# Optimization experiments

Measured on AMD Instinct MI355X. Metric: run time of the kernel, lower is better.

Reference implementation:

```python
import jax, jax.numpy as jnp
import numpy as np

N = 20000      # nodes
E = 80000      # edges (before self loops)
NG = 64        # graphs in batch
EMB = 780      # embedding_size (768 text + 12 time)
NEG_SLOPE = 0.2
BN_EPS = 1e-5


def setup_inputs() -> dict:
    key = jax.random.key(0)
    ks = jax.random.split(key, 20)
    def rn(k, shape, s=0.05):
        return jax.random.normal(k, shape, dtype=jnp.float32) * s
    z = lambda n: jnp.zeros((n,), dtype=jnp.float32)
    o = lambda n: jnp.ones((n,), dtype=jnp.float32)
    x = jax.random.normal(ks[0], (N, 772), dtype=jnp.float32)
    edge_index = jax.random.randint(ks[1], (2, E), 0, N)
    batch = jnp.sort(jax.random.randint(ks[2], (N,), 0, NG))
    return dict(
        x=x, edge_index=edge_index, batch=batch,
        time_W=rn(ks[3], (4, 12)), time_b=z(12),
        lin_W0=rn(ks[4], (EMB, 3 * EMB)), att_src0=rn(ks[5], (3, EMB)), att_dst0=rn(ks[6], (3, EMB)),
        bias0=z(3 * EMB), gamma0=o(3 * EMB), beta0=z(3 * EMB),
        lin_W1=rn(ks[7], (3 * EMB, 3 * EMB)), att_src1=rn(ks[8], (3, EMB)), att_dst1=rn(ks[9], (3, EMB)),
        bias1=z(3 * EMB), gamma1=o(3 * EMB), beta1=z(3 * EMB),
        lin_W2=rn(ks[10], (3 * EMB, EMB)), att_src2=rn(ks[11], (1, EMB)), att_dst2=rn(ks[12], (1, EMB)),
        bias2=z(EMB), gamma2=o(EMB), beta2=z(EMB),
        mlp_W1=rn(ks[13], (EMB, 128)), mlp_b1=z(128),
        mlp_W2=rn(ks[14], (128, 64)), mlp_b2=z(64),
    )


def _gat_layer(h, src, dst, W, a_src, a_dst, b, heads):
    # PyG GATConv (eval mode: dropout off), concat=True, self loops already in src/dst
    C = W.shape[1] // heads
    hp = (h @ W).reshape(N, heads, C)                       # [N,H,C]
    a_s = jnp.sum(hp * a_src[None], axis=-1)                # [N,H]
    a_d = jnp.sum(hp * a_dst[None], axis=-1)                # [N,H]
    e = jax.nn.leaky_relu(a_s[src] + a_d[dst], NEG_SLOPE)   # [E+N,H]
    m = jax.ops.segment_max(e, dst, num_segments=N)         # segment softmax over incoming edges
    m = jnp.where(jnp.isfinite(m), m, 0.0)
    p = jnp.exp(e - m[dst])
    denom = jax.ops.segment_sum(p, dst, num_segments=N)
    alpha = p / (denom[dst] + 1e-16)                        # [E+N,H]
    out = jax.ops.segment_sum(alpha[:, :, None] * hp[src], dst, num_segments=N)  # [N,H,C]
    return out.reshape(N, heads * C) + b


def _bn(h, gamma, beta):
    # BatchNorm in training-mode math (batch statistics, biased variance)
    mu = jnp.mean(h, axis=0)
    var = jnp.mean((h - mu) ** 2, axis=0)
    return (h - mu) * jax.lax.rsqrt(var + BN_EPS) * gamma + beta


def reference(x, edge_index, batch, time_W, time_b,
              lin_W0, att_src0, att_dst0, bias0, gamma0, beta0,
              lin_W1, att_src1, att_dst1, bias1, gamma1, beta1,
              lin_W2, att_src2, att_dst2, bias2, gamma2, beta2,
              mlp_W1, mlp_b1, mlp_W2, mlp_b2):
    te = x[:, 768:772] @ time_W + time_b
    h = jnp.concatenate([jax.lax.stop_gradient(x[:, :768]), te,
                         jax.lax.stop_gradient(x[:, 772:])], axis=-1)  # [N, 780]
    sl = jnp.arange(N)
    src = jnp.concatenate([edge_index[0], sl])   # add self loops
    dst = jnp.concatenate([edge_index[1], sl])
    layers = [
        (lin_W0, att_src0, att_dst0, bias0, gamma0, beta0, 3),
        (lin_W1, att_src1, att_dst1, bias1, gamma1, beta1, 3),
        (lin_W2, att_src2, att_dst2, bias2, gamma2, beta2, 1),
    ]
    for W, a_s, a_d, b, g, bt, heads in layers:
        h = jnp.tanh(_gat_layer(h, src, dst, W, a_s, a_d, b, heads))
        h = _bn(h, g, bt)
    cnt = jax.ops.segment_sum(jnp.ones((N,), dtype=h.dtype), batch, num_segments=NG)
    pooled = jax.ops.segment_sum(h, batch, num_segments=NG) / jnp.maximum(cnt, 1.0)[:, None]
    pooled = jax.nn.relu(pooled)
    out = jnp.tanh(pooled @ mlp_W1 + mlp_b1) @ mlp_W2 + mlp_b2
    return out  # [NG, 64]
```

## Files before the change

### kernel.cpp

```cpp
#include <hip/hip_runtime.h>
#include <math.h>

#define NN   20000
#define EE   80000
#define ELP  100000
#define NGR  64
#define EMB  780
#define W3   2340
#define EMBP 832
#define W3P  2368
#define NZ   (W3+8)

static inline int cdiv_i(long long a, long long b){ return (int)((a + b - 1) / b); }

typedef _Float16 f16;
typedef _Float16 f16x4 __attribute__((ext_vector_type(4)));
typedef _Float16 f16x8 __attribute__((ext_vector_type(8)));
typedef float    f32x4 __attribute__((ext_vector_type(4)));

__device__ __forceinline__ void async_ld16(const f16* g, f16* l){
    __builtin_amdgcn_global_load_lds(
        (const __attribute__((address_space(1))) unsigned int*)g,
        (__attribute__((address_space(3))) unsigned int*)l,
        16, 0, 0);
}

__global__ void k_zero_f32(float* p, int n){
    int i = blockIdx.x*256 + threadIdx.x; if (i < n) p[i] = 0.f;
}
__global__ void k_zero_i32(int* p, int n){
    int i = blockIdx.x*256 + threadIdx.x; if (i < n) p[i] = 0;
}

__global__ void k_transpose(const float* __restrict__ W, f16* __restrict__ Wt,
                            const float* __restrict__ sc, const float* __restrict__ sh,
                            float* __restrict__ dvec, int K, int N, int KP){
    __shared__ float T[32][33];
    __shared__ float D[8][33];
    int n0 = blockIdx.x*32, k0 = blockIdx.y*32;
    int tx = threadIdx.x, ty = threadIdx.y;
    float raw[4];
#pragma unroll
    for (int r = 0; r < 4; r++){
        int k = k0 + ty + r*8;
        float w = 0.f;
        if (k < K && n0 + tx < N) w = W[(size_t)k*N + n0 + tx];
        raw[r] = w;
        T[ty + r*8][tx] = sc ? w * ((k < K) ? sc[k] : 0.f) : w;
    }
    if (sh){
        float p = 0.f;
#pragma unroll
        for (int r = 0; r < 4; r++){
            int k = k0 + ty + r*8;
            if (k < K) p += sh[k] * raw[r];
        }
        D[ty][tx] = p;
    }
    __syncthreads();
#pragma unroll
    for (int r = 0; r < 4; r++){
        int n = n0 + ty + r*8;
        int k = k0 + tx;
        if (n < N && k < KP) Wt[(size_t)n*KP + k] = (f16)T[tx][ty + r*8];
    }
    if (sh && ty == 0 && n0 + tx < N){
        float s = 0.f;
#pragma unroll
        for (int j = 0; j < 8; j++) s += D[j][tx];
        atomicAdd(&dvec[n0 + tx], s);
    }
}

__global__ void k_wvec(const float* __restrict__ W, const float* __restrict__ asrc,
                       const float* __restrict__ adst, const float* __restrict__ sc,
                       f16* __restrict__ Wt, float* __restrict__ dvec,
                       int K, int N, int KP, int H){
    int k = blockIdx.x*4 + (threadIdx.x >> 6);
    int lane = threadIdx.x & 63;
    if (k < K){
        const float* row = W + (size_t)k*N;
        float acc[6];
#pragma unroll
        for (int i = 0; i < 6; i++) acc[i] = 0.f;
        for (int c = lane; c < EMB; c += 64){
            for (int h = 0; h < H; h++){
                float wv = row[h*EMB + c];
                acc[h]     += wv * asrc[h*EMB + c];
                acc[H + h] += wv * adst[h*EMB + c];
            }
        }
        float s = sc ? sc[k] : 1.f;
        for (int i = 0; i < 2*H; i++){
            float v = acc[i];
#pragma unroll
            for (int off = 32; off; off >>= 1) v += __shfl_xor(v, off);
            if (lane == 0) Wt[(size_t)(N + i)*KP + k] = (f16)(v * s);
        }
    }
    if (blockIdx.x == 0){
        int wv = threadIdx.x >> 6;
        for (int i = wv; i < 2*H; i += 4){
            int h = (i < H) ? i : (i - H);
            const float* att = (i < H) ? (asrc + h*EMB) : (adst + h*EMB);
            float s = 0.f;
            for (int c = lane; c < EMB; c += 64) s += dvec[h*EMB + c] * att[c];
#pragma unroll
            for (int off = 32; off; off >>= 1) s += __shfl_xor(s, off);
            if (lane == 0) dvec[N + i] = s;
        }
    }
}

__global__ void k_build_h(const float* __restrict__ x, const float* __restrict__ tW,
                          const float* __restrict__ tb, f16* __restrict__ h){
    int idx = blockIdx.x*256 + threadIdx.x;
    int total = NN*(EMBP/4);
    if (idx >= total) return;
    int n = idx / (EMBP/4);
    int c0 = (idx - n*(EMBP/4))*4;
    const float* xr = x + (size_t)n*772;
    f16x4 o;
#pragma unroll
    for (int j = 0; j < 4; j++){
        int c = c0 + j; float v;
        if (c < 768) v = xr[c];
        else if (c < EMB){
            int t = c - 768;
            v = tb[t] + xr[768]*tW[t] + xr[769]*tW[12+t] + xr[770]*tW[24+t] + xr[771]*tW[36+t];
        } else v = 0.f;
        o[j] = (f16)v;
    }
    *(f16x4*)(h + (size_t)n*EMBP + c0) = o;
}

__global__ void k_deg(const int* __restrict__ ei, int* __restrict__ deg){
    int k = blockIdx.x*256 + threadIdx.x; if (k >= ELP) return;
    int d = (k < EE) ? ei[EE + k] : (k - EE);
    atomicAdd(&deg[d], 1);
}

__global__ __launch_bounds__(1024) void k_scan(int* __restrict__ deg, int* __restrict__ rp){
    __shared__ int part[1024];
    int tid = threadIdx.x;
    int i0 = tid*20;
    int n = (i0 < NN) ? min(20, NN - i0) : 0;
    int s = 0;
    for (int k = 0; k < n; k++) s += deg[i0+k];
    part[tid] = s; __syncthreads();
    for (int off = 1; off < 1024; off <<= 1){
        int t = (tid >= off) ? part[tid-off] : 0;
        __syncthreads();
        part[tid] += t;
        __syncthreads();
    }
    int run = part[tid] - s;
    for (int k = 0; k < n; k++){
        int d = deg[i0+k];
        rp[i0+k] = run;
        deg[i0+k] = run;
        run += d;
    }
    if (tid == 1023) rp[NN] = part[1023];
}

__global__ void k_fill(const int* __restrict__ ei, int* __restrict__ cursor, int* __restrict__ csrc){
    int k = blockIdx.x*256 + threadIdx.x; if (k >= ELP) return;
    int s, d;
    if (k < EE){ s = ei[k]; d = ei[EE + k]; } else { s = k - EE; d = s; }
    int pos = atomicAdd(&cursor[d], 1);
    csrc[pos] = s;
}

__global__ void k_grp(const int* __restrict__ batch, int* __restrict__ grp){
    int g = blockIdx.x*256 + threadIdx.x; if (g > NGR) return;
    int lo = 0, hi = NN;
    while (lo < hi){ int mid = (lo+hi)>>1; if (batch[mid] < g) lo = mid+1; else hi = mid; }
    grp[g] = lo;
}

__global__ __launch_bounds__(512, 4) void k_gemmT(const f16* __restrict__ A,
                                                  const f16* __restrict__ Bt,
                                                  const float* __restrict__ dvec,
                                                  f16* __restrict__ C,
                                                  float* __restrict__ a_sd,
                                                  int M, int N, int NB, int H,
                                                  int KP, int SN, int Mtiles, int NT){
    __shared__ f16 smem[36864];
    f16* sB = smem + 12288;

    int nwg = Mtiles*NT;
    int bid = blockIdx.x;
    int q = nwg >> 3, r = nwg & 7, xcd = bid & 7, lin = bid >> 3;
    int wg = (xcd < r ? xcd*(q+1) : r*(q+1) + (xcd - r)*q) + lin;
    int mt = wg / NT, nt = wg - mt*NT;
    int m0 = mt*128, n0 = nt*256;

    int tid = threadIdx.x;
    int w = tid >> 6, lane = tid & 63;
    int lm = lane & 15, lq = lane >> 4;
    int wm = w >> 2, wn = w & 3;

    int kqs = ((lane & 3) ^ ((lane >> 3) & 3)) * 8;
    const f16* gA0 = A  + (size_t)min(m0 + w*16 + (lane >> 2), M-1)*KP + kqs;
    const f16* gB0 = Bt + (size_t)min(n0 + w*32 + (lane >> 2), NB-1)*KP + kqs;
    const f16* gB1 = Bt + (size_t)min(n0 + w*32 + 16 + (lane >> 2), NB-1)*KP + kqs;
    int sa0 = w*512;
    int sb0 = w*1024, sb1 = w*1024 + 512;

    int swz  = (lq ^ ((lm >> 1) & 3)) * 8;
    int aoff = (wm*64 + lm)*32 + swz;
    int boff = (wn*64 + lm)*32 + swz;

    f32x4 acc[4][4];
#pragma unroll
    for (int i = 0; i < 4; i++)
#pragma unroll
        for (int j = 0; j < 4; j++) acc[i][j] = (f32x4)0.f;

    int KT = KP >> 5;

    async_ld16(gA0,      &smem[sa0]);
    async_ld16(gB0,      &sB[sb0]);
    async_ld16(gB1,      &sB[sb1]);
    async_ld16(gA0 + 32, &smem[4096 + sa0]);
    async_ld16(gB0 + 32, &sB[8192 + sb0]);
    async_ld16(gB1 + 32, &sB[8192 + sb1]);
    asm volatile("s_waitcnt vmcnt(3)" ::: "memory");
    __builtin_amdgcn_s_barrier();

    int cur = 0, nx2 = 2;
    for (int t = 0; t < KT; t++){
        int ac = cur*4096, bc = cur*8192;
        f16x8 aF[4], bF[4];
#pragma unroll
        for (int i = 0; i < 4; i++) aF[i] = *(const f16x8*)&smem[ac + aoff + i*512];
#pragma unroll
        for (int i = 0; i < 4; i++) bF[i] = *(const f16x8*)&sB[bc + boff + i*512];
        bool s2 = (t+2 < KT);
        if (s2){
            int ko2 = (t+2)*32;
            int a2 = nx2*4096, b2 = nx2*8192;
            async_ld16(gA0 + ko2, &smem[a2 + sa0]);
            async_ld16(gB0 + ko2, &sB[b2 + sb0]);
            async_ld16(gB1 + ko2, &sB[b2 + sb1]);
        }
        __builtin_amdgcn_s_setprio(1);
#pragma unroll
        for (int i = 0; i < 4; i++)
#pragma unroll
            for (int j = 0; j < 4; j++)
                acc[i][j] = __builtin_amdgcn_mfma_f32_16x16x32_f16(aF[i], bF[j], acc[i][j], 0, 0, 0);
        __builtin_amdgcn_s_setprio(0);
        if (s2) asm volatile("s_waitcnt vmcnt(3)" ::: "memory");
        else    asm volatile("s_waitcnt vmcnt(0)" ::: "memory");
        __builtin_amdgcn_s_barrier();
        cur = (cur == 2) ? 0 : cur + 1;
        nx2 = (nx2 == 2) ? 0 : nx2 + 1;
    }

#pragma unroll
    for (int mi = 0; mi < 4; mi++){
#pragma unroll
        for (int ni = 0; ni < 4; ni++){
            int col = n0 + wn*64 + ni*16 + lm;
            if (col >= N && col < NB){
                int jc = col - N;
                int idx = (jc < H) ? jc : (3 + jc - H);
                float dv = dvec[col];
                int rbase = m0 + wm*64 + mi*16 + lq*4;
#pragma unroll
                for (int rr = 0; rr < 4; rr++){
                    int row = rbase + rr;
                    if (row < M) a_sd[(size_t)row*6 + idx] = acc[mi][ni][rr] + dv;
                }
            }
        }
    }

    float dv4[4];
#pragma unroll
    for (int ni = 0; ni < 4; ni++){
        int gcol = n0 + wn*64 + ni*16 + lm;
        dv4[ni] = (gcol < N) ? dvec[gcol] : 0.f;
    }
    int ncols = min(256, N - n0);
#pragma unroll
    for (int mi = 0; mi < 4; mi++){
#pragma unroll
        for (int ni = 0; ni < 4; ni++){
            int colL = wn*64 + ni*16 + lm;
#pragma unroll
            for (int rr = 0; rr < 4; rr++){
                int rowL = wm*64 + mi*16 + lq*4 + rr;
                smem[rowL*264 + colL] = (f16)(acc[mi][ni][rr] + dv4[ni]);
            }
        }
    }
    asm volatile("s_waitcnt lgkmcnt(0)" ::: "memory");
    __builtin_amdgcn_s_barrier();
#pragma unroll
    for (int it = 0; it < 8; it++){
        int ch = tid + it*512;
        int rowL = ch >> 5, cc = (ch & 31)*8;
        int grow = m0 + rowL;
        if (grow < M && cc < ncols){
            if (cc + 8 <= ncols){
                f16x8 v = *(f16x8*)&smem[rowL*264 + cc];
                *(f16x8*)(C + (size_t)grow*SN + n0 + cc) = v;
            } else {
                for (int jj = cc; jj < ncols; jj++)
                    C[(size_t)grow*SN + n0 + jj] = smem[rowL*264 + jj];
            }
        }
    }
}

template<int H>
__global__ __launch_bounds__(256) void k_alpha(const int* __restrict__ rp, const int* __restrict__ csrc,
                                               const float* __restrict__ a_sd, float* __restrict__ alpha){
    int n = blockIdx.x*4 + (threadIdx.x >> 6);
    if (n >= NN) return;
    int lane = threadIdx.x & 63;
    int beg = rp[n], deg = rp[n+1] - beg;

    float adv[H];
#pragma unroll
    for (int h = 0; h < H; h++) adv[h] = a_sd[(size_t)n*6 + 3 + h];

    bool act0 = lane < deg;
    int sl0 = 0; float t0[H];
    if (act0){
        sl0 = csrc[beg + lane];
#pragma unroll
        for (int h = 0; h < H; h++){
            float t = a_sd[(size_t)sl0*6 + h] + adv[h];
            t0[h] = t > 0.f ? t : 0.2f*t;
        }
    } else {
#pragma unroll
        for (int h = 0; h < H; h++) t0[h] = -1e30f;
    }

    float mx[H];
#pragma unroll
    for (int h = 0; h < H; h++) mx[h] = t0[h];
    for (int base = 64; base < deg; base += 64){
        int e = base + lane;
        if (e < deg){
            int s = csrc[beg + e];
#pragma unroll
            for (int h = 0; h < H; h++){
                float t = a_sd[(size_t)s*6 + h] + adv[h];
                t = t > 0.f ? t : 0.2f*t;
                mx[h] = fmaxf(mx[h], t);
            }
        }
    }
#pragma unroll
    for (int off = 32; off; off >>= 1)
#pragma unroll
        for (int h = 0; h < H; h++) mx[h] = fmaxf(mx[h], __shfl_xor(mx[h], off));

    float dn[H];
#pragma unroll
    for (int h = 0; h < H; h++) dn[h] = act0 ? expf(t0[h] - mx[h]) : 0.f;
    for (int base = 64; base < deg; base += 64){
        int e = base + lane;
        if (e < deg){
            int s = csrc[beg + e];
#pragma unroll
            for (int h = 0; h < H; h++){
                float t = a_sd[(size_t)s*6 + h] + adv[h];
                t = t > 0.f ? t : 0.2f*t;
                dn[h] += expf(t - mx[h]);
            }
        }
    }
#pragma unroll
    for (int off = 32; off; off >>= 1)
#pragma unroll
        for (int h = 0; h < H; h++) dn[h] += __shfl_xor(dn[h], off);
    float inv[H];
#pragma unroll
    for (int h = 0; h < H; h++) inv[h] = 1.f / (dn[h] + 1e-16f);

    if (act0){
        if (H == 3){
            float4 o;
            o.x = expf(t0[0]-mx[0])*inv[0];
            o.y = expf(t0[1]-mx[1])*inv[1];
            o.z = expf(t0[2]-mx[2])*inv[2];
            o.w = 0.f;
            *(float4*)(alpha + (size_t)(beg+lane)*4) = o;
        } else {
            alpha[beg+lane] = expf(t0[0]-mx[0])*inv[0];
        }
    }
    for (int base = 64; base < deg; base += 64){
        int e = base + lane;
        if (e < deg){
            int s = csrc[beg + e];
            float av[H];
#pragma unroll
            for (int h = 0; h < H; h++){
                float t = a_sd[(size_t)s*6 + h] + adv[h];
                t = t > 0.f ? t : 0.2f*t;
                av[h] = expf(t - mx[h]) * inv[h];
            }
            if (H == 3){
                float4 o; o.x = av[0]; o.y = av[1]; o.z = av[2]; o.w = 0.f;
                *(float4*)(alpha + (size_t)(beg+e)*4) = o;
            } else {
                alpha[beg+e] = av[0];
            }
        }
    }
}

template<int H>
__global__ __launch_bounds__(256) void k_gather(const f16* __restrict__ hp, const int* __restrict__ rp,
                                                const int* __restrict__ csrc, const float* __restrict__ alpha,
                                                const float* __restrict__ bias, f16* __restrict__ y,
                                                int SP, int W){
    int w = threadIdx.x >> 6, lane = threadIdx.x & 63;
    int n = blockIdx.x*4 + w;
    if (n >= NN) return;
    int c = blockIdx.y*512 + lane*8;
    bool cok = c < SP;
    int beg = rp[n], deg = rp[n+1] - beg;

    int hl = 0, hh = 0, nsp = 8;
    if (H == 3){
        hl = min(c/EMB, 2); hh = min((c+7)/EMB, 2);
        nsp = (hh > hl) ? (EMB*(hl+1) - c) : 8;
    }
    float acc[8];
#pragma unroll
    for (int j = 0; j < 8; j++) acc[j] = 0.f;

    for (int base = 0; base < deg; base += 64){
        int cnt = min(64, deg - base);
        int e0 = base + lane;
        int sl = 0; float a0v = 0.f, a1v = 0.f, a2v = 0.f;
        if (e0 < deg){
            sl = csrc[beg + e0];
            if (H == 3){
                float4 al4 = *(const float4*)(alpha + (size_t)(beg+e0)*4);
                a0v = al4.x; a1v = al4.y; a2v = al4.z;
            } else {
                a0v = alpha[beg + e0];
            }
        }
#pragma unroll 4
        for (int e = 0; e < cnt; e++){
            int s = __shfl(sl, e);
            float b0 = __shfl(a0v, e);
            float b1 = (H==3) ? __shfl(a1v, e) : b0;
            float b2 = (H==3) ? __shfl(a2v, e) : b0;
            if (cok){
                f16x8 v = *(const f16x8*)(hp + (size_t)s*SP + c);
                float lo = (H==3) ? ((hl==0)?b0:((hl==1)?b1:b2)) : b0;
                float hi = (H==3) ? ((hh==0)?b0:((hh==1)?b1:b2)) : b0;
#pragma unroll
                for (int j = 0; j < 8; j++)
                    acc[j] += ((j < nsp) ? lo : hi) * (float)v[j];
            }
        }
    }

    if (cok){
        f16x8 o;
#pragma unroll
        for (int j = 0; j < 8; j++){
            float vv = (c + j < W) ? tanhf(acc[j] + bias[c+j]) : 0.f;
            o[j] = (f16)vv;
        }
        *(f16x8*)(y + (size_t)n*SP + c) = o;
    }
}

__global__ void k_bnstat(const f16* __restrict__ y, float* __restrict__ ps,
                         float* __restrict__ pq, int W, int SP){
    int c0 = (blockIdx.x*256 + threadIdx.x)*4;
    if (c0 >= W) return;
    int slice = blockIdx.y;
    int r0 = (int)(((long long)NN*slice)/128);
    int r1 = (int)(((long long)NN*(slice+1))/128);
    float s[4] = {0,0,0,0}, q[4] = {0,0,0,0};
    for (int r = r0; r < r1; r++){
        f16x4 u = *(const f16x4*)(y + (size_t)r*SP + c0);
#pragma unroll
        for (int j = 0; j < 4; j++){ float v = (float)u[j]; s[j] += v; q[j] += v*v; }
    }
#pragma unroll
    for (int j = 0; j < 4; j++){
        ps[(size_t)slice*W3 + c0+j] = s[j];
        pq[(size_t)slice*W3 + c0+j] = q[j];
    }
}

__global__ void k_bnfin(const float* __restrict__ ps, const float* __restrict__ pq,
                        const float* __restrict__ gamma, const float* __restrict__ beta,
                        float* __restrict__ sc, float* __restrict__ sh,
                        float* __restrict__ dvec, int W, int zn){
    int c = blockIdx.x*256 + threadIdx.x;
    if (c < W){
        float m = 0.f, q = 0.f;
        for (int s = 0; s < 128; s++){ m += ps[(size_t)s*W3 + c]; q += pq[(size_t)s*W3 + c]; }
        m *= (1.f/NN);
        float v = q * (1.f/NN) - m*m;
        float is = 1.f / sqrtf(v + 1e-5f);
        float g = gamma[c];
        sc[c] = is * g;
        sh[c] = beta[c] - m * is * g;
    }
    if (c < zn) dvec[c] = 0.f;
}

__global__ void k_pool(const f16* __restrict__ h, const int* __restrict__ grp,
                       float* __restrict__ pooled){
    int g = blockIdx.x;
    int c = threadIdx.x*4;
    if (c >= EMB) return;
    int r0 = grp[g], r1 = grp[g+1];
    float s0=0.f, s1=0.f, s2=0.f, s3=0.f;
    for (int r = r0; r < r1; r++){
        f16x4 u = *(const f16x4*)(h + (size_t)r*EMBP + c);
        s0 += (float)u[0]; s1 += (float)u[1]; s2 += (float)u[2]; s3 += (float)u[3];
    }
    pooled[g*EMB + c] = s0; pooled[g*EMB + c+1] = s1;
    pooled[g*EMB + c+2] = s2; pooled[g*EMB + c+3] = s3;
}

__global__ __launch_bounds__(256) void k_mlp(const float* __restrict__ pooled, const int* __restrict__ grp,
                                             const float* __restrict__ sc, const float* __restrict__ sh,
                                             const float* __restrict__ W1, const float* __restrict__ b1,
                                             const float* __restrict__ W2, const float* __restrict__ b2,
                                             float* __restrict__ out){
    __shared__ float p[EMB];
    __shared__ float hid[128];
    int g = blockIdx.x, tid = threadIdx.x;
    int cnt = grp[g+1] - grp[g];
    float ic = 1.f / fmaxf((float)cnt, 1.f);
    for (int c = tid; c < EMB; c += 256){
        float v = pooled[g*EMB + c] * ic * sc[c] + sh[c];
        p[c] = v > 0.f ? v : 0.f;
    }
    __syncthreads();
    if (tid < 128){
        float s = b1[tid];
        for (int k = 0; k < EMB; k++) s += p[k] * W1[k*128 + tid];
        hid[tid] = tanhf(s);
    }
    __syncthreads();
    if (tid < 64){
        float s = b2[tid];
        for (int k = 0; k < 128; k++) s += hid[k] * W2[k*64 + tid];
        out[g*64 + tid] = s;
    }
}

extern "C" void kernel_launch(void* const* d_in, const int* in_sizes, int n_in,
                              void* d_out, int out_size, void* d_ws, size_t ws_size,
                              hipStream_t stream) {
    (void)in_sizes; (void)n_in; (void)out_size;
    const float* x    = (const float*)d_in[0];
    const int*   ei   = (const int*)  d_in[1];
    const int*   batch= (const int*)  d_in[2];
    const float* tW   = (const float*)d_in[3];
    const float* tb   = (const float*)d_in[4];
    const float* W0   = (const float*)d_in[5];
    const float* as0  = (const float*)d_in[6];
    const float* ad0  = (const float*)d_in[7];
    const float* b0   = (const float*)d_in[8];
    const float* g0   = (const float*)d_in[9];
    const float* be0  = (const float*)d_in[10];
    const float* W1   = (const float*)d_in[11];
    const float* as1  = (const float*)d_in[12];
    const float* ad1  = (const float*)d_in[13];
    const float* b1   = (const float*)d_in[14];
    const float* g1   = (const float*)d_in[15];
    const float* be1  = (const float*)d_in[16];
    const float* W2   = (const float*)d_in[17];
    const float* as2  = (const float*)d_in[18];
    const float* ad2  = (const float*)d_in[19];
    const float* b2   = (const float*)d_in[20];
    const float* g2   = (const float*)d_in[21];
    const float* be2  = (const float*)d_in[22];
    const float* mW1  = (const float*)d_in[23];
    const float* mb1  = (const float*)d_in[24];
    const float* mW2  = (const float*)d_in[25];
    const float* mb2  = (const float*)d_in[26];
    float* outp = (float*)d_out;

    size_t off = 0;
    auto carve = [&](size_t bytes) -> void* {
        void* p = (char*)d_ws + off;
        off = (off + bytes + 255) & ~(size_t)255;
        return p;
    };
    f16* big1 = (f16*)carve((size_t)NN*W3P*2);
    f16* big2 = (f16*)carve((size_t)NN*W3P*2);
    f16* Wt   = (f16*)carve((size_t)NZ*W3P*2);
    float* a_sd  = (float*)carve((size_t)NN*6*4);
    float* psum  = (float*)carve((size_t)128*W3*4);
    float* psq   = (float*)carve((size_t)128*W3*4);
    float* sc    = (float*)carve((size_t)W3*4);
    float* sh    = (float*)carve((size_t)W3*4);
    float* dvec  = (float*)carve((size_t)NZ*4);
    float* alphab= (float*)carve((size_t)ELP*4*4);
    float* pooled= (float*)carve((size_t)NGR*EMB*4);
    int*   grp   = (int*)carve((size_t)(NGR+1)*4);
    int*   deg   = (int*)carve((size_t)NN*4);
    int*   rp    = (int*)carve((size_t)(NN+1)*4);
    int*   csrc  = (int*)carve((size_t)ELP*4);

    if (ws_size < off) return;

    k_zero_i32<<<cdiv_i(NN,256),256,0,stream>>>(deg, NN);
    k_deg<<<cdiv_i(ELP,256),256,0,stream>>>(ei, deg);
    k_scan<<<1,1024,0,stream>>>(deg, rp);
    k_fill<<<cdiv_i(ELP,256),256,0,stream>>>(ei, deg, csrc);
    k_grp<<<1,256,0,stream>>>(batch, grp);

    k_build_h<<<cdiv_i((long long)NN*(EMBP/4),256),256,0,stream>>>(x, tW, tb, big1);
    k_zero_f32<<<cdiv_i(NZ,256),256,0,stream>>>(dvec, NZ);

    struct Layer { const float* W; const float* as; const float* ad; const float* b;
                   const float* g; const float* be; int H; int K; int KP; };
    Layer layers[3] = {
        {W0, as0, ad0, b0, g0, be0, 3, EMB, EMBP},
        {W1, as1, ad1, b1, g1, be1, 3, W3,  W3P },
        {W2, as2, ad2, b2, g2, be2, 1, W3,  W3P },
    };

    for (int L = 0; L < 3; L++){
        Layer& ly = layers[L];
        int Wout  = ly.H * EMB;
        int NB    = Wout + 2*ly.H;
        int SPout = (Wout == W3) ? W3P : EMBP;
        const float* scale = (L == 0) ? nullptr : sc;
        const float* shift = (L == 0) ? nullptr : sh;

        dim3 tg(cdiv_i(Wout,32), cdiv_i(ly.KP,32));
        k_transpose<<<tg, dim3(32,8), 0, stream>>>(ly.W, Wt, scale, shift, dvec, ly.K, Wout, ly.KP);
        k_wvec<<<cdiv_i(ly.K,4),256,0,stream>>>(ly.W, ly.as, ly.ad, scale, Wt, dvec, ly.K, Wout, ly.KP, ly.H);

        int Mtiles = cdiv_i(NN,128), NT = cdiv_i(NB,256);
        k_gemmT<<<Mtiles*NT, 512, 0, stream>>>(big1, Wt, dvec, big2, a_sd,
                                               NN, Wout, NB, ly.H, ly.KP, SPout, Mtiles, NT);

        dim3 gg(cdiv_i(NN,4), cdiv_i(SPout,512));
        if (ly.H == 3){
            k_alpha<3><<<cdiv_i(NN,4),256,0,stream>>>(rp, csrc, a_sd, alphab);
            k_gather<3><<<gg,256,0,stream>>>(big2, rp, csrc, alphab, ly.b, big1, SPout, Wout);
        } else {
            k_alpha<1><<<cdiv_i(NN,4),256,0,stream>>>(rp, csrc, a_sd, alphab);
            k_gather<1><<<gg,256,0,stream>>>(big2, rp, csrc, alphab, ly.b, big1, SPout, Wout);
        }

        dim3 gs(cdiv_i(Wout/4,256), 128);
        k_bnstat<<<gs,256,0,stream>>>(big1, psum, psq, Wout, SPout);
        int zn = (L < 2) ? NZ : 0;
        k_bnfin<<<cdiv_i(Wout,256),256,0,stream>>>(psum, psq, ly.g, ly.be, sc, sh, dvec, Wout, zn);
    }

    k_pool<<<NGR,256,0,stream>>>(big1, grp, pooled);
    k_mlp<<<NGR,256,0,stream>>>(pooled, grp, sc, sh, mW1, mb1, mW2, mb2, outp);
}
```

Baseline: 1.400 ms.

## Add small-tile GEMM for last layer and LDS-prefetched edge gather

Adds a 128x128-tile, 256-thread GEMM variant with triple-buffered async LDS loads. It is used only for the third layer, whose narrow output of 782 columns fills the 256-wide tiles poorly. The edge gather now runs through a per-wave LDS ring: each wave issues async global-to-LDS loads of neighbor rows four edges ahead and waits with vmcnt, so the loads of upcoming edges overlap the accumulation of the current one. The trade-offs are extra LDS use per block, which can lower occupancy, and tighter waitcnt logic with more risk of mistakes.

```diff
diff --git a/kernel.cpp b/kernel.cpp
--- a/kernel.cpp
+++ b/kernel.cpp
@@ -316,6 +316,141 @@
     }
 }
 
+__global__ __launch_bounds__(256, 3) void k_gemmS(const f16* __restrict__ A,
+                                                  const f16* __restrict__ Bt,
+                                                  const float* __restrict__ dvec,
+                                                  f16* __restrict__ C,
+                                                  float* __restrict__ a_sd,
+                                                  int M, int N, int NB, int H,
+                                                  int KP, int SN, int Mtiles, int NT){
+    __shared__ f16 smem[24576];
+    f16* sB = smem + 12288;
+
+    int nwg = Mtiles*NT;
+    int bid = blockIdx.x;
+    int q = nwg >> 3, r = nwg & 7, xcd = bid & 7, lin = bid >> 3;
+    int wg = (xcd < r ? xcd*(q+1) : r*(q+1) + (xcd - r)*q) + lin;
+    int mt = wg / NT, nt = wg - mt*NT;
+    int m0 = mt*128, n0 = nt*128;
+
+    int tid = threadIdx.x;
+    int w = tid >> 6, lane = tid & 63;
+    int lm = lane & 15, lq = lane >> 4;
+    int wm = w >> 1, wn = w & 1;
+
+    int kqs = ((lane & 3) ^ ((lane >> 3) & 3)) * 8;
+    const f16* gA0 = A  + (size_t)min(m0 + w*32 + (lane >> 2), M-1)*KP + kqs;
+    const f16* gA1 = A  + (size_t)min(m0 + w*32 + 16 + (lane >> 2), M-1)*KP + kqs;
+    const f16* gB0 = Bt + (size_t)min(n0 + w*32 + (lane >> 2), NB-1)*KP + kqs;
+    const f16* gB1 = Bt + (size_t)min(n0 + w*32 + 16 + (lane >> 2), NB-1)*KP + kqs;
+    int sa0 = w*1024, sa1 = w*1024 + 512;
+    int sb0 = w*1024, sb1 = w*1024 + 512;
+
+    int swz  = (lq ^ ((lm >> 1) & 3)) * 8;
+    int aoff = (wm*64 + lm)*32 + swz;
+    int boff = (wn*64 + lm)*32 + swz;
+
+    f32x4 acc[4][4];
+#pragma unroll
+    for (int i = 0; i < 4; i++)
+#pragma unroll
+        for (int j = 0; j < 4; j++) acc[i][j] = (f32x4)0.f;
+
+    int KT = KP >> 5;
+
+    async_ld16(gA0,      &smem[sa0]);        async_ld16(gA1,      &smem[sa1]);
+    async_ld16(gB0,      &sB[sb0]);          async_ld16(gB1,      &sB[sb1]);
+    async_ld16(gA0 + 32, &smem[4096 + sa0]); async_ld16(gA1 + 32, &smem[4096 + sa1]);
+    async_ld16(gB0 + 32, &sB[4096 + sb0]);   async_ld16(gB1 + 32, &sB[4096 + sb1]);
+    asm volatile("s_waitcnt vmcnt(4)" ::: "memory");
+    __builtin_amdgcn_s_barrier();
+
+    int cur = 0, nx2 = 2;
+    for (int t = 0; t < KT; t++){
+        int ac = cur*4096, bc = cur*4096;
+        f16x8 aF[4], bF[4];
+#pragma unroll
+        for (int i = 0; i < 4; i++) aF[i] = *(const f16x8*)&smem[ac + aoff + i*512];
+#pragma unroll
+        for (int i = 0; i < 4; i++) bF[i] = *(const f16x8*)&sB[bc + boff + i*512];
+        bool s2 = (t+2 < KT);
+        if (s2){
+            int ko2 = (t+2)*32;
+            int a2 = nx2*4096, b2 = nx2*4096;
+            async_ld16(gA0 + ko2, &smem[a2 + sa0]); async_ld16(gA1 + ko2, &smem[a2 + sa1]);
+            async_ld16(gB0 + ko2, &sB[b2 + sb0]);   async_ld16(gB1 + ko2, &sB[b2 + sb1]);
+        }
+        __builtin_amdgcn_s_setprio(1);
+#pragma unroll
+        for (int i = 0; i < 4; i++)
+#pragma unroll
+            for (int j = 0; j < 4; j++)
+                acc[i][j] = __builtin_amdgcn_mfma_f32_16x16x32_f16(aF[i], bF[j], acc[i][j], 0, 0, 0);
+        __builtin_amdgcn_s_setprio(0);
+        if (s2) asm volatile("s_waitcnt vmcnt(4)" ::: "memory");
+        else    asm volatile("s_waitcnt vmcnt(0)" ::: "memory");
+        __builtin_amdgcn_s_barrier();
+        cur = (cur == 2) ? 0 : cur + 1;
+        nx2 = (nx2 == 2) ? 0 : nx2 + 1;
+    }
+
+#pragma unroll
+    for (int mi = 0; mi < 4; mi++){
+#pragma unroll
+        for (int ni = 0; ni < 4; ni++){
+            int col = n0 + wn*64 + ni*16 + lm;
+            if (col >= N && col < NB){
+                int jc = col - N;
+                int idx = (jc < H) ? jc : (3 + jc - H);
+                float dv = dvec[col];
+                int rbase = m0 + wm*64 + mi*16 + lq*4;
+#pragma unroll
+                for (int rr = 0; rr < 4; rr++){
+                    int row = rbase + rr;
+                    if (row < M) a_sd[(size_t)row*6 + idx] = acc[mi][ni][rr] + dv;
+                }
+            }
+        }
+    }
+
+    float dv4[4];
+#pragma unroll
+    for (int ni = 0; ni < 4; ni++){
+        int gcol = n0 + wn*64 + ni*16 + lm;
+        dv4[ni] = (gcol < N) ? dvec[gcol] : 0.f;
+    }
+    int ncols = min(128, N - n0);
+#pragma unroll
+    for (int mi = 0; mi < 4; mi++){
+#pragma unroll
+        for (int ni = 0; ni < 4; ni++){
+            int colL = wn*64 + ni*16 + lm;
+#pragma unroll
+            for (int rr = 0; rr < 4; rr++){
+                int rowL = wm*64 + mi*16 + lq*4 + rr;
+                smem[rowL*136 + colL] = (f16)(acc[mi][ni][rr] + dv4[ni]);
+            }
+        }
+    }
+    asm volatile("s_waitcnt lgkmcnt(0)" ::: "memory");
+    __builtin_amdgcn_s_barrier();
+#pragma unroll
+    for (int it = 0; it < 8; it++){
+        int ch = tid + it*256;
+        int rowL = ch >> 4, cc = (ch & 15)*8;
+        int grow = m0 + rowL;
+        if (grow < M && cc < ncols){
+            if (cc + 8 <= ncols){
+                f16x8 v = *(f16x8*)&smem[rowL*136 + cc];
+                *(f16x8*)(C + (size_t)grow*SN + n0 + cc) = v;
+            } else {
+                for (int jj = cc; jj < ncols; jj++)
+                    C[(size_t)grow*SN + n0 + jj] = smem[rowL*136 + jj];
+            }
+        }
+    }
+}
+
 template<int H>
 __global__ __launch_bounds__(256) void k_alpha(const int* __restrict__ rp, const int* __restrict__ csrc,
                                                const float* __restrict__ a_sd, float* __restrict__ alpha){
@@ -419,16 +554,19 @@
 }
 
 template<int H>
-__global__ __launch_bounds__(256) void k_gather(const f16* __restrict__ hp, const int* __restrict__ rp,
-                                                const int* __restrict__ csrc, const float* __restrict__ alpha,
-                                                const float* __restrict__ bias, f16* __restrict__ y,
-                                                int SP, int W){
+__global__ __launch_bounds__(256) void k_gather2(const f16* __restrict__ hp, const int* __restrict__ rp,
+                                                 const int* __restrict__ csrc, const float* __restrict__ alpha,
+                                                 const float* __restrict__ bias, f16* __restrict__ y,
+                                                 int SP, int W){
+    __shared__ f16 ring[12288];
     int w = threadIdx.x >> 6, lane = threadIdx.x & 63;
     int n = blockIdx.x*4 + w;
     if (n >= NN) return;
-    int c = blockIdx.y*512 + lane*8;
+    int cb = blockIdx.y*512;
+    int c = cb + lane*8;
     bool cok = c < SP;
     int beg = rp[n], deg = rp[n+1] - beg;
+    f16* slot = ring + w*3072;
 
     int hl = 0, hh = 0, nsp = 8;
     if (H == 3){
@@ -439,33 +577,64 @@
 #pragma unroll
     for (int j = 0; j < 8; j++) acc[j] = 0.f;
 
+    const f16* hpc = hp + cb + lane*8;
+
     for (int base = 0; base < deg; base += 64){
         int cnt = min(64, deg - base);
-        int e0 = base + lane;
-        int sl = 0; float a0v = 0.f, a1v = 0.f, a2v = 0.f;
-        if (e0 < deg){
-            sl = csrc[beg + e0];
+        int e = base + lane;
+        int sl = 0; float a0 = 0.f, a1 = 0.f, a2 = 0.f;
+        if (e < deg){
+            sl = csrc[beg + e];
             if (H == 3){
-                float4 al4 = *(const float4*)(alpha + (size_t)(beg+e0)*4);
-                a0v = al4.x; a1v = al4.y; a2v = al4.z;
+                float4 q = *(const float4*)(alpha + (size_t)(beg+e)*4);
+                a0 = q.x; a1 = q.y; a2 = q.z;
             } else {
-                a0v = alpha[beg + e0];
-            }
-        }
-#pragma unroll 4
-        for (int e = 0; e < cnt; e++){
-            int s = __shfl(sl, e);
-            float b0 = __shfl(a0v, e);
-            float b1 = (H==3) ? __shfl(a1v, e) : b0;
-            float b2 = (H==3) ? __shfl(a2v, e) : b0;
+                a0 = alpha[beg + e];
+            }
+        }
+        int P = min(4, cnt);
+        for (int j = 0; j < P; j++){
+            int s = __shfl(sl, j);
+            async_ld16(hpc + (size_t)s*SP, slot + j*512);
+        }
+        int M = cnt - 4; if (M < 0) M = 0;
+        int rc = 0, ri = 4;
+        for (int j = 0; j < M; j++){
+            asm volatile("s_waitcnt vmcnt(3)" ::: "memory");
+            f16x8 v = *(const f16x8*)(slot + rc*512 + lane*8);
+            float b0 = __shfl(a0, j);
+            float lo, hi;
+            if (H == 3){
+                float b1 = __shfl(a1, j), b2 = __shfl(a2, j);
+                lo = (hl==0)?b0:((hl==1)?b1:b2);
+                hi = (hh==0)?b0:((hh==1)?b1:b2);
+            } else { lo = b0; hi = b0; }
             if (cok){
-                f16x8 v = *(const f16x8*)(hp + (size_t)s*SP + c);
-                float lo = (H==3) ? ((hl==0)?b0:((hl==1)?b1:b2)) : b0;
-                float hi = (H==3) ? ((hh==0)?b0:((hh==1)?b1:b2)) : b0;
-#pragma unroll
-                for (int j = 0; j < 8; j++)
-                    acc[j] += ((j < nsp) ? lo : hi) * (float)v[j];
-            }
+#pragma unroll
+                for (int jj = 0; jj < 8; jj++)
+                    acc[jj] += ((jj < nsp) ? lo : hi) * (float)v[jj];
+            }
+            int s2 = __shfl(sl, j+4);
+            async_ld16(hpc + (size_t)s2*SP, slot + ri*512);
+            rc = (rc == 5) ? 0 : rc + 1;
+            ri = (ri == 5) ? 0 : ri + 1;
+        }
+        asm volatile("s_waitcnt vmcnt(0)" ::: "memory");
+        for (int j = M; j < cnt; j++){
+            f16x8 v = *(const f16x8*)(slot + rc*512 + lane*8);
+            float b0 = __shfl(a0, j);
+            float lo, hi;
+            if (H == 3){
+                float b1 = __shfl(a1, j), b2 = __shfl(a2, j);
+                lo = (hl==0)?b0:((hl==1)?b1:b2);
+                hi = (hh==0)?b0:((hh==1)?b1:b2);
+            } else { lo = b0; hi = b0; }
+            if (cok){
+#pragma unroll
+                for (int jj = 0; jj < 8; jj++)
+                    acc[jj] += ((jj < nsp) ? lo : hi) * (float)v[jj];
+            }
+            rc = (rc == 5) ? 0 : rc + 1;
         }
     }
 
@@ -647,17 +816,23 @@
         k_transpose<<<tg, dim3(32,8), 0, stream>>>(ly.W, Wt, scale, shift, dvec, ly.K, Wout, ly.KP);
         k_wvec<<<cdiv_i(ly.K,4),256,0,stream>>>(ly.W, ly.as, ly.ad, scale, Wt, dvec, ly.K, Wout, ly.KP, ly.H);
 
-        int Mtiles = cdiv_i(NN,128), NT = cdiv_i(NB,256);
-        k_gemmT<<<Mtiles*NT, 512, 0, stream>>>(big1, Wt, dvec, big2, a_sd,
-                                               NN, Wout, NB, ly.H, ly.KP, SPout, Mtiles, NT);
+        if (L < 2){
+            int Mtiles = cdiv_i(NN,128), NT = cdiv_i(NB,256);
+            k_gemmT<<<Mtiles*NT, 512, 0, stream>>>(big1, Wt, dvec, big2, a_sd,
+                                                   NN, Wout, NB, ly.H, ly.KP, SPout, Mtiles, NT);
+        } else {
+            int Mtiles = cdiv_i(NN,128), NT = cdiv_i(NB,128);
+            k_gemmS<<<Mtiles*NT, 256, 0, stream>>>(big1, Wt, dvec, big2, a_sd,
+                                                   NN, Wout, NB, ly.H, ly.KP, SPout, Mtiles, NT);
+        }
 
         dim3 gg(cdiv_i(NN,4), cdiv_i(SPout,512));
         if (ly.H == 3){
             k_alpha<3><<<cdiv_i(NN,4),256,0,stream>>>(rp, csrc, a_sd, alphab);
-            k_gather<3><<<gg,256,0,stream>>>(big2, rp, csrc, alphab, ly.b, big1, SPout, Wout);
+            k_gather2<3><<<gg,256,0,stream>>>(big2, rp, csrc, alphab, ly.b, big1, SPout, Wout);
         } else {
             k_alpha<1><<<cdiv_i(NN,4),256,0,stream>>>(rp, csrc, a_sd, alphab);
-            k_gather<1><<<gg,256,0,stream>>>(big2, rp, csrc, alphab, ly.b, big1, SPout, Wout);
+            k_gather2<1><<<gg,256,0,stream>>>(big2, rp, csrc, alphab, ly.b, big1, SPout, Wout);
         }
 
         dim3 gs(cdiv_i(Wout/4,256), 128);
```

Result: slower. 1.481 ms (+5.8%).
